# Performance work log

Measured on AMD Instinct MI355X. Metric: run time of the kernel, lower is better.

The kernel has to match this reference:

```python
import jax, jax.numpy as jnp
import numpy as np

EPS = 1e-6
ROPE_THETA = 10000.0


def setup_inputs() -> dict:
    key = jax.random.key(0)
    ks = jax.random.split(key, 6)
    B, S, D = 2, 2048, 2048
    H, KVH, HD = 16, 4, 128
    hidden_states = jax.random.normal(ks[0], (B, S, D), dtype=jnp.float32)
    # RoPE tables (HF style: freqs duplicated across the two halves)
    inv_freq = 1.0 / (ROPE_THETA ** (jnp.arange(0, HD, 2, dtype=jnp.float32) / HD))
    pos = jnp.arange(S, dtype=jnp.float32)
    freqs = pos[:, None] * inv_freq[None, :]            # [S, HD/2]
    emb = jnp.concatenate([freqs, freqs], axis=-1)       # [S, HD]
    cos, sin = jnp.cos(emb), jnp.sin(emb)
    w_scale = 0.02
    q_w = jax.random.normal(ks[1], (H * HD, D), dtype=jnp.float32) * w_scale
    k_w = jax.random.normal(ks[2], (KVH * HD, D), dtype=jnp.float32) * w_scale
    v_w = jax.random.normal(ks[3], (KVH * HD, D), dtype=jnp.float32) * w_scale
    o_w = jax.random.normal(ks[4], (D, H * HD), dtype=jnp.float32) * w_scale
    q_norm_w = jnp.ones((HD,), dtype=jnp.float32)
    k_norm_w = jnp.ones((HD,), dtype=jnp.float32)
    return {
        "hidden_states": hidden_states, "cos": cos, "sin": sin,
        "q_w": q_w, "k_w": k_w, "v_w": v_w, "o_w": o_w,
        "q_norm_w": q_norm_w, "k_norm_w": k_norm_w,
    }


def _rms_norm(x, w):
    # Qwen3RMSNorm: fp32 variance, scale, cast back
    xf = x.astype(jnp.float32)
    var = jnp.mean(xf * xf, axis=-1, keepdims=True)
    out = xf * jax.lax.rsqrt(var + EPS)
    return (out * w.astype(jnp.float32)).astype(x.dtype)


def _rotate_half(x):
    half = x.shape[-1] // 2
    return jnp.concatenate([-x[..., half:], x[..., :half]], axis=-1)


def reference(hidden_states, cos, sin, q_w, k_w, v_w, o_w, q_norm_w, k_norm_w):
    B, S, D = hidden_states.shape
    HD = q_norm_w.shape[0]
    H = q_w.shape[0] // HD
    KVH = k_w.shape[0] // HD
    groups = H // KVH
    scale = HD ** -0.5

    # QKV projections (no bias) -> [B, heads, S, HD]
    q = (hidden_states @ q_w.T).reshape(B, S, H, HD)
    k = (hidden_states @ k_w.T).reshape(B, S, KVH, HD)
    v = (hidden_states @ v_w.T).reshape(B, S, KVH, HD)
    q = _rms_norm(q, q_norm_w).transpose(0, 2, 1, 3)   # [B,H,S,HD]
    k = _rms_norm(k, k_norm_w).transpose(0, 2, 1, 3)   # [B,KVH,S,HD]
    v = v.transpose(0, 2, 1, 3)                        # [B,KVH,S,HD]

    # RoPE (broadcast over batch and heads)
    c = cos[None, None, :, :]
    s = sin[None, None, :, :]
    q = q * c + _rotate_half(q) * s
    k = k * c + _rotate_half(k) * s

    # GQA expand kv heads
    if groups > 1:
        k = jnp.repeat(k, groups, axis=1)              # [B,H,S,HD]
        v = jnp.repeat(v, groups, axis=1)

    # SDPA, non-causal, no mask, no dropout
    scores = jnp.einsum("bhqd,bhkd->bhqk", q, k) * scale
    probs = jax.nn.softmax(scores, axis=-1)
    attn = jnp.einsum("bhqk,bhkd->bhqd", probs, v)     # [B,H,S,HD]

    attn = attn.transpose(0, 2, 1, 3).reshape(B, S, H * HD)
    return attn @ o_w.T
```

## Files before the change

kernel.cpp:

```cpp
#include <hip/hip_runtime.h>
#include <hip/hip_bf16.h>
#include <math.h>

#define B_   2
#define S_   2048
#define D_   2048
#define H_   16
#define KVH_ 4
#define HD_  128
#define SCALE 0.08838834764831845f

typedef unsigned short u16;
typedef __attribute__((ext_vector_type(8))) short bf16x8;
typedef __attribute__((ext_vector_type(4))) float f32x4;

__device__ __forceinline__ u16 f2bf(float x) {
    union { float f; unsigned int u; } v; v.f = x;
    unsigned int r = v.u + 0x7fffu + ((v.u >> 16) & 1u);
    return (u16)(r >> 16);
}
__device__ __forceinline__ float bf2f(u16 b) {
    union { float f; unsigned int u; } v; v.u = ((unsigned int)b) << 16;
    return v.f;
}
__device__ __forceinline__ void gload16(const void* g, void* lds) {
    __builtin_amdgcn_global_load_lds(
        (const __attribute__((address_space(1))) unsigned int*)g,
        (__attribute__((address_space(3))) unsigned int*)lds, 16, 0, 0);
}

__global__ __launch_bounds__(256) void f2b_kernel(
    const float* __restrict__ s, u16* __restrict__ d, int n4)
{
    int i = blockIdx.x * 256 + threadIdx.x;
    if (i >= n4) return;
    float4 v = ((const float4*)s)[i];
    ushort4 o = make_ushort4(f2bf(v.x), f2bf(v.y), f2bf(v.z), f2bf(v.w));
    ((ushort4*)d)[i] = o;
}

template<int MODE>
__global__ __launch_bounds__(256) void gemm_bf16(
    const u16* __restrict__ A,
    const u16* __restrict__ Bw,
    u16* __restrict__ Qo, u16* __restrict__ Ko, u16* __restrict__ Vt,
    float* __restrict__ Co)
{
    __shared__ u16 As[128 * 64];
    __shared__ u16 Bs[128 * 64];

    const int t  = threadIdx.x;
    const int w  = t >> 6, l = t & 63;
    const int wm = w >> 1, wn = w & 1;
    const int lr = l & 15, lh = l >> 4;
    const int n0 = blockIdx.x * 128;
    const int m0 = blockIdx.y * 128;

    f32x4 acc[4][4];
    #pragma unroll
    for (int i = 0; i < 4; ++i)
        #pragma unroll
        for (int j = 0; j < 4; ++j)
            acc[i][j] = (f32x4)0.f;

    const int x  = (w * 4) * 1024 + l * 16;
    for (int k0 = 0; k0 < 2048; k0 += 64) {
        #pragma unroll
        for (int u = 0; u < 4; ++u) {
            int xb = x + u * 1024;
            int r  = xb >> 7;
            int c  = xb & 127;
            int cs = c ^ ((r & 7) << 4);
            gload16(&A[(size_t)(m0 + r) * 2048 + k0 + (cs >> 1)], &As[(w * 4 + u) * 512]);
            gload16(&Bw[(size_t)(n0 + r) * 2048 + k0 + (cs >> 1)], &Bs[(w * 4 + u) * 512]);
        }
        __syncthreads();
        #pragma unroll
        for (int kc = 0; kc < 2; ++kc) {
            bf16x8 af[4], bfr[4];
            #pragma unroll
            for (int i = 0; i < 4; ++i) {
                int row = wm * 64 + i * 16 + lr;
                int byt = row * 128 + ((kc * 64 + lh * 16) ^ ((row & 7) << 4));
                af[i] = *(const bf16x8*)&As[byt >> 1];
                int rob = wn * 64 + i * 16 + lr;
                int byb = rob * 128 + ((kc * 64 + lh * 16) ^ ((rob & 7) << 4));
                bfr[i] = *(const bf16x8*)&Bs[byb >> 1];
            }
            #pragma unroll
            for (int i = 0; i < 4; ++i)
                #pragma unroll
                for (int j = 0; j < 4; ++j)
                    acc[i][j] = __builtin_amdgcn_mfma_f32_16x16x32_bf16(
                        af[i], bfr[j], acc[i][j], 0, 0, 0);
        }
        __syncthreads();
    }

    #pragma unroll
    for (int i = 0; i < 4; ++i) {
        #pragma unroll
        for (int j = 0; j < 4; ++j) {
            int col = n0 + wn * 64 + j * 16 + lr;
            #pragma unroll
            for (int r = 0; r < 4; ++r) {
                int m = m0 + wm * 64 + i * 16 + lh * 4 + r;
                float v = acc[i][j][r];
                if (MODE == 0) {
                    int bb = m >> 11, s = m & 2047;
                    if (col < 2048) {
                        int hh = col >> 7, d = col & 127;
                        Qo[((size_t)(bb * H_ + hh) * S_ + s) * HD_ + d] = f2bf(v);
                    } else if (col < 2560) {
                        int c2 = col - 2048; int hh = c2 >> 7, d = c2 & 127;
                        Ko[((size_t)(bb * KVH_ + hh) * S_ + s) * HD_ + d] = f2bf(v);
                    } else {
                        int c2 = col - 2560; int hh = c2 >> 7, d = c2 & 127;
                        Vt[((size_t)(bb * KVH_ + hh) * HD_ + d) * S_ + s] = f2bf(v);
                    }
                } else {
                    Co[(size_t)m * 2048 + col] = v;
                }
            }
        }
    }
}

__global__ __launch_bounds__(256) void norm_rope(
    u16* __restrict__ Qb, u16* __restrict__ Kb,
    const float* __restrict__ cosb, const float* __restrict__ sinb,
    const float* __restrict__ qnw, const float* __restrict__ knw)
{
    const int rid = blockIdx.x * 4 + (threadIdx.x >> 6);
    const int l   = threadIdx.x & 63;
    u16* row; const float* wn; int s; float sc;
    if (rid < B_ * H_ * S_) {
        row = Qb + (size_t)rid * HD_; wn = qnw; s = rid & (S_ - 1); sc = SCALE;
    } else {
        int r2 = rid - B_ * H_ * S_;
        row = Kb + (size_t)r2 * HD_; wn = knw; s = r2 & (S_ - 1); sc = 1.f;
    }
    unsigned int u = *(const unsigned int*)&row[2 * l];
    float x0 = bf2f((u16)(u & 0xffff)), x1 = bf2f((u16)(u >> 16));
    float ss = x0 * x0 + x1 * x1;
    #pragma unroll
    for (int off = 1; off < 64; off <<= 1) ss += __shfl_xor(ss, off);
    float rr = rsqrtf(ss * (1.f / 128.f) + 1e-6f);
    float n0 = x0 * rr * wn[2 * l];
    float n1 = x1 * rr * wn[2 * l + 1];
    float p0 = __shfl_xor(n0, 32);
    float p1 = __shfl_xor(n1, 32);
    float sg = (l < 32) ? -1.f : 1.f;
    const float* cp = cosb + s * HD_;
    const float* sp = sinb + s * HD_;
    float o0 = (n0 * cp[2 * l]     + sg * p0 * sp[2 * l])     * sc;
    float o1 = (n1 * cp[2 * l + 1] + sg * p1 * sp[2 * l + 1]) * sc;
    unsigned int o = (unsigned int)f2bf(o0) | ((unsigned int)f2bf(o1) << 16);
    *(unsigned int*)&row[2 * l] = o;
}

__global__ __launch_bounds__(256, 2) void attn_mfma(
    const u16* __restrict__ Q,
    const u16* __restrict__ K,
    const u16* __restrict__ Vt,
    u16* __restrict__ AO)
{
    __shared__ u16 Ks[64 * 128];
    __shared__ u16 Vs[128 * 64];
    __shared__ u16 Ps[4][32 * 72];

    const int t = threadIdx.x, w = t >> 6, l = t & 63;
    const int lr = l & 15, lh = l >> 4;
    const int bh = blockIdx.y;
    const int bb = bh >> 4, h = bh & 15;
    const int kv = bb * KVH_ + (h >> 2);
    const int q0 = blockIdx.x * 128 + w * 32;

    const u16* Qp = Q + ((size_t)bh * S_ + q0) * HD_;
    const u16* Kp = K + (size_t)kv * S_ * HD_;
    const u16* Vp = Vt + (size_t)kv * HD_ * S_;

    bf16x8 aq[2][4];
    #pragma unroll
    for (int rb = 0; rb < 2; ++rb)
        #pragma unroll
        for (int dc = 0; dc < 4; ++dc)
            aq[rb][dc] = *(const bf16x8*)&Qp[(size_t)(rb * 16 + lr) * 128 + dc * 32 + lh * 8];

    f32x4 oacc[2][8];
    #pragma unroll
    for (int rb = 0; rb < 2; ++rb)
        #pragma unroll
        for (int db = 0; db < 8; ++db)
            oacc[rb][db] = (f32x4)0.f;
    float mrun[2][4], lrun[2][4];
    #pragma unroll
    for (int rb = 0; rb < 2; ++rb)
        #pragma unroll
        for (int r = 0; r < 4; ++r) { mrun[rb][r] = -1e30f; lrun[rb][r] = 0.f; }

    for (int kt = 0; kt < S_ / 64; ++kt) {
        const int k0 = kt * 64;
        #pragma unroll
        for (int u = 0; u < 4; ++u) {
            int xb = (w * 4 + u) * 1024 + l * 16;
            int rk = xb >> 8, ck = xb & 255;
            gload16(&Kp[(size_t)(k0 + rk) * 128 + ((ck ^ ((rk & 7) << 4)) >> 1)],
                    &Ks[(w * 4 + u) * 512]);
            int rv = xb >> 7, cv = xb & 127;
            gload16(&Vp[(size_t)rv * S_ + k0 + ((cv ^ ((rv & 7) << 4)) >> 1)],
                    &Vs[(w * 4 + u) * 512]);
        }
        __syncthreads();

        f32x4 sacc[2][4];
        #pragma unroll
        for (int rb = 0; rb < 2; ++rb)
            #pragma unroll
            for (int kb = 0; kb < 4; ++kb) sacc[rb][kb] = (f32x4)0.f;
        #pragma unroll
        for (int kb = 0; kb < 4; ++kb) {
            bf16x8 kf[4];
            #pragma unroll
            for (int dc = 0; dc < 4; ++dc) {
                int row = kb * 16 + lr;
                int byt = row * 256 + ((dc * 64 + lh * 16) ^ ((row & 7) << 4));
                kf[dc] = *(const bf16x8*)&Ks[byt >> 1];
            }
            #pragma unroll
            for (int rb = 0; rb < 2; ++rb)
                #pragma unroll
                for (int dc = 0; dc < 4; ++dc)
                    sacc[rb][kb] = __builtin_amdgcn_mfma_f32_16x16x32_bf16(
                        aq[rb][dc], kf[dc], sacc[rb][kb], 0, 0, 0);
        }

        #pragma unroll
        for (int rb = 0; rb < 2; ++rb) {
            #pragma unroll
            for (int r = 0; r < 4; ++r) {
                float mx = fmaxf(fmaxf(sacc[rb][0][r], sacc[rb][1][r]),
                                 fmaxf(sacc[rb][2][r], sacc[rb][3][r]));
                mx = fmaxf(mx, __shfl_xor(mx, 1));
                mx = fmaxf(mx, __shfl_xor(mx, 2));
                mx = fmaxf(mx, __shfl_xor(mx, 4));
                mx = fmaxf(mx, __shfl_xor(mx, 8));
                float mo = mrun[rb][r];
                float mn = fmaxf(mo, mx);
                float al = __expf(mo - mn);
                mrun[rb][r] = mn;
                float ps = 0.f;
                #pragma unroll
                for (int kb = 0; kb < 4; ++kb) {
                    float p = __expf(sacc[rb][kb][r] - mn);
                    sacc[rb][kb][r] = p;
                    ps += p;
                }
                ps += __shfl_xor(ps, 1);
                ps += __shfl_xor(ps, 2);
                ps += __shfl_xor(ps, 4);
                ps += __shfl_xor(ps, 8);
                lrun[rb][r] = lrun[rb][r] * al + ps;
                #pragma unroll
                for (int db = 0; db < 8; ++db)
                    oacc[rb][db][r] *= al;
                int prow = rb * 16 + lh * 4 + r;
                #pragma unroll
                for (int kb = 0; kb < 4; ++kb)
                    Ps[w][prow * 72 + kb * 16 + lr] = f2bf(sacc[rb][kb][r]);
            }
        }
        asm volatile("s_waitcnt lgkmcnt(0)" ::: "memory");

        #pragma unroll
        for (int kc = 0; kc < 2; ++kc) {
            bf16x8 pf[2];
            #pragma unroll
            for (int rb = 0; rb < 2; ++rb)
                pf[rb] = *(const bf16x8*)&Ps[w][(rb * 16 + lr) * 72 + kc * 32 + lh * 8];
            #pragma unroll
            for (int db = 0; db < 8; ++db) {
                int row = db * 16 + lr;
                int byt = row * 128 + ((kc * 64 + lh * 16) ^ ((row & 7) << 4));
                bf16x8 vf = *(const bf16x8*)&Vs[byt >> 1];
                #pragma unroll
                for (int rb = 0; rb < 2; ++rb)
                    oacc[rb][db] = __builtin_amdgcn_mfma_f32_16x16x32_bf16(
                        pf[rb], vf, oacc[rb][db], 0, 0, 0);
            }
        }
        __syncthreads();
    }

    #pragma unroll
    for (int rb = 0; rb < 2; ++rb) {
        #pragma unroll
        for (int r = 0; r < 4; ++r) {
            float inv = 1.f / lrun[rb][r];
            int s = q0 + rb * 16 + lh * 4 + r;
            size_t base = ((size_t)bb * S_ + s) * 2048 + h * 128;
            #pragma unroll
            for (int db = 0; db < 8; ++db)
                AO[base + db * 16 + lr] = f2bf(oacc[rb][db][r] * inv);
        }
    }
}

extern "C" void kernel_launch(void* const* d_in, const int* in_sizes, int n_in,
                              void* d_out, int out_size, void* d_ws, size_t ws_size,
                              hipStream_t stream) {
    (void)in_sizes; (void)n_in; (void)out_size; (void)ws_size;
    const float* hid  = (const float*)d_in[0];
    const float* cosb = (const float*)d_in[1];
    const float* sinb = (const float*)d_in[2];
    const float* qw   = (const float*)d_in[3];
    const float* kw   = (const float*)d_in[4];
    const float* vw   = (const float*)d_in[5];
    const float* ow   = (const float*)d_in[6];
    const float* qnw  = (const float*)d_in[7];
    const float* knw  = (const float*)d_in[8];

    u16* ws   = (u16*)d_ws;
    u16* hidB = ws;
    u16* Wc   = ws + 8388608;
    u16* owB  = ws + 14680064;
    u16* Qb   = ws + 18874368;
    u16* Kb   = ws + 27262976;
    u16* VtB  = ws + 29360128;
    u16* AO   = ws + 31457280;

    f2b_kernel<<<8192, 256, 0, stream>>>(hid, hidB, 2097152);
    f2b_kernel<<<4096, 256, 0, stream>>>(qw, Wc, 1048576);
    f2b_kernel<<<1024, 256, 0, stream>>>(kw, Wc + 4194304, 262144);
    f2b_kernel<<<1024, 256, 0, stream>>>(vw, Wc + 5242880, 262144);
    f2b_kernel<<<4096, 256, 0, stream>>>(ow, owB, 1048576);

    gemm_bf16<0><<<dim3(24, 32), 256, 0, stream>>>(hidB, Wc, Qb, Kb, VtB, nullptr);
    norm_rope<<<20480, 256, 0, stream>>>(Qb, Kb, cosb, sinb, qnw, knw);
    attn_mfma<<<dim3(16, 32), 256, 0, stream>>>(Qb, Kb, VtB, AO);
    gemm_bf16<1><<<dim3(16, 32), 256, 0, stream>>>(AO, owB, nullptr, nullptr, nullptr,
                                                   (float*)d_out);
}
```

Baseline: 278.0 us.

## Rewrite attention with 32x32 MFMA, register-resident P, double buffering, lazy rescale

Rebuilds the attention kernel around 32x32x16 MFMA with transposed S=K·Q^T so each lane owns one query column. P is packed to bf16 with v_cvt_pk_bf16_f32 and moved by cross-lane shuffles instead of an LDS round trip. K/V tiles are double-buffered so the next tile's loads overlap compute. Softmax works in base-2, with log2e folded into the Q scale, and skips rescaling the accumulator unless the max grows by more than 8. Block IDs are remapped to group blocks that share KV heads, at the cost of more LDS per block and higher register pressure.

```diff
diff --git a/kernel.cpp b/kernel.cpp
--- a/kernel.cpp
+++ b/kernel.cpp
@@ -9,10 +9,13 @@
 #define KVH_ 4
 #define HD_  128
 #define SCALE 0.08838834764831845f
+#define LOG2E 1.44269504088896f
 
 typedef unsigned short u16;
-typedef __attribute__((ext_vector_type(8))) short bf16x8;
-typedef __attribute__((ext_vector_type(4))) float f32x4;
+typedef unsigned int   u32;
+typedef __attribute__((ext_vector_type(8)))  short bf16x8;
+typedef __attribute__((ext_vector_type(4)))  float f32x4;
+typedef __attribute__((ext_vector_type(16))) float f32x16;
 
 __device__ __forceinline__ u16 f2bf(float x) {
     union { float f; unsigned int u; } v; v.f = x;
@@ -22,6 +25,11 @@
 __device__ __forceinline__ float bf2f(u16 b) {
     union { float f; unsigned int u; } v; v.u = ((unsigned int)b) << 16;
     return v.f;
+}
+__device__ __forceinline__ u32 cvtpk(float lo, float hi) {
+    u32 r;
+    asm("v_cvt_pk_bf16_f32 %0, %1, %2" : "=v"(r) : "v"(lo), "v"(hi));
+    return r;
 }
 __device__ __forceinline__ void gload16(const void* g, void* lds) {
     __builtin_amdgcn_global_load_lds(
@@ -135,7 +143,7 @@
     const int l   = threadIdx.x & 63;
     u16* row; const float* wn; int s; float sc;
     if (rid < B_ * H_ * S_) {
-        row = Qb + (size_t)rid * HD_; wn = qnw; s = rid & (S_ - 1); sc = SCALE;
+        row = Qb + (size_t)rid * HD_; wn = qnw; s = rid & (S_ - 1); sc = SCALE * LOG2E;
     } else {
         int r2 = rid - B_ * H_ * S_;
         row = Kb + (size_t)r2 * HD_; wn = knw; s = r2 & (S_ - 1); sc = 1.f;
@@ -165,144 +173,137 @@
     const u16* __restrict__ Vt,
     u16* __restrict__ AO)
 {
-    __shared__ u16 Ks[64 * 128];
-    __shared__ u16 Vs[128 * 64];
-    __shared__ u16 Ps[4][32 * 72];
-
-    const int t = threadIdx.x, w = t >> 6, l = t & 63;
-    const int lr = l & 15, lh = l >> 4;
-    const int bh = blockIdx.y;
+    __shared__ u16 Ks[2][64 * 128];
+    __shared__ u16 Vs[2][128 * 64];
+
+    const int t  = threadIdx.x, w = t >> 6, l = t & 63;
+    const int lq = l & 31, hi = l >> 5;
+    const int id = (blockIdx.x & 7) * 64 + (blockIdx.x >> 3);
+    const int qx = id & 15, bh = id >> 4;
     const int bb = bh >> 4, h = bh & 15;
     const int kv = bb * KVH_ + (h >> 2);
-    const int q0 = blockIdx.x * 128 + w * 32;
+    const int q0 = qx * 128 + w * 32;
 
     const u16* Qp = Q + ((size_t)bh * S_ + q0) * HD_;
     const u16* Kp = K + (size_t)kv * S_ * HD_;
     const u16* Vp = Vt + (size_t)kv * HD_ * S_;
 
-    bf16x8 aq[2][4];
-    #pragma unroll
-    for (int rb = 0; rb < 2; ++rb)
-        #pragma unroll
-        for (int dc = 0; dc < 4; ++dc)
-            aq[rb][dc] = *(const bf16x8*)&Qp[(size_t)(rb * 16 + lr) * 128 + dc * 32 + lh * 8];
-
-    f32x4 oacc[2][8];
-    #pragma unroll
-    for (int rb = 0; rb < 2; ++rb)
-        #pragma unroll
-        for (int db = 0; db < 8; ++db)
-            oacc[rb][db] = (f32x4)0.f;
-    float mrun[2][4], lrun[2][4];
-    #pragma unroll
-    for (int rb = 0; rb < 2; ++rb)
-        #pragma unroll
-        for (int r = 0; r < 4; ++r) { mrun[rb][r] = -1e30f; lrun[rb][r] = 0.f; }
-
-    for (int kt = 0; kt < S_ / 64; ++kt) {
-        const int k0 = kt * 64;
+    bf16x8 aq[8];
+    #pragma unroll
+    for (int ks = 0; ks < 8; ++ks)
+        aq[ks] = *(const bf16x8*)&Qp[(size_t)lq * 128 + ks * 16 + hi * 8];
+
+    f32x16 oacc[4];
+    #pragma unroll
+    for (int dt = 0; dt < 4; ++dt) oacc[dt] = (f32x16)0.f;
+    float mrun = -1e30f, lrun = 0.f;
+
+    auto stage = [&](int k0, int buf) {
         #pragma unroll
         for (int u = 0; u < 4; ++u) {
             int xb = (w * 4 + u) * 1024 + l * 16;
             int rk = xb >> 8, ck = xb & 255;
             gload16(&Kp[(size_t)(k0 + rk) * 128 + ((ck ^ ((rk & 7) << 4)) >> 1)],
-                    &Ks[(w * 4 + u) * 512]);
+                    &Ks[buf][(w * 4 + u) * 512]);
             int rv = xb >> 7, cv = xb & 127;
             gload16(&Vp[(size_t)rv * S_ + k0 + ((cv ^ ((rv & 7) << 4)) >> 1)],
-                    &Vs[(w * 4 + u) * 512]);
+                    &Vs[buf][(w * 4 + u) * 512]);
+        }
+    };
+
+    stage(0, 0);
+    __syncthreads();
+
+    const int NT = S_ / 64;
+    for (int kt = 0; kt < NT; ++kt) {
+        const int cur = kt & 1;
+        if (kt + 1 < NT) stage((kt + 1) * 64, cur ^ 1);
+
+        f32x16 sacc[2];
+        sacc[0] = (f32x16)0.f; sacc[1] = (f32x16)0.f;
+        #pragma unroll
+        for (int kb = 0; kb < 2; ++kb) {
+            #pragma unroll
+            for (int ks = 0; ks < 8; ++ks) {
+                int row = kb * 32 + lq;
+                int byt = row * 256 + ((ks * 32 + hi * 16) ^ ((row & 7) << 4));
+                bf16x8 kf = *(const bf16x8*)&Ks[cur][byt >> 1];
+                sacc[kb] = __builtin_amdgcn_mfma_f32_32x32x16_bf16(
+                    kf, aq[ks], sacc[kb], 0, 0, 0);
+            }
+        }
+
+        float mx = -1e30f;
+        #pragma unroll
+        for (int kb = 0; kb < 2; ++kb)
+            #pragma unroll
+            for (int r = 0; r < 16; ++r)
+                mx = fmaxf(mx, sacc[kb][r]);
+        mx = fmaxf(mx, __shfl_xor(mx, 32));
+        if (__any(mx > mrun + 8.f)) {
+            float mn = fmaxf(mrun, mx);
+            float al = __builtin_exp2f(mrun - mn);
+            mrun = mn;
+            lrun *= al;
+            #pragma unroll
+            for (int r = 0; r < 16; ++r) {
+                int src = (r & 3) + 8 * (r >> 2) + 4 * hi;
+                float alr = __shfl(al, src);
+                #pragma unroll
+                for (int dt = 0; dt < 4; ++dt) oacc[dt][r] *= alr;
+            }
+        }
+        float ps = 0.f;
+        #pragma unroll
+        for (int kb = 0; kb < 2; ++kb)
+            #pragma unroll
+            for (int r = 0; r < 16; ++r) {
+                float p = __builtin_exp2f(sacc[kb][r] - mrun);
+                sacc[kb][r] = p;
+                ps += p;
+            }
+        ps += __shfl_xor(ps, 32);
+        lrun += ps;
+
+        #pragma unroll
+        for (int kb = 0; kb < 2; ++kb) {
+            u32 wv[8], sv[8];
+            #pragma unroll
+            for (int i = 0; i < 8; ++i)
+                wv[i] = cvtpk(sacc[kb][2 * i], sacc[kb][2 * i + 1]);
+            #pragma unroll
+            for (int i = 0; i < 8; ++i)
+                sv[i] = __shfl_xor(wv[i], 32);
+            #pragma unroll
+            for (int k2 = 0; k2 < 2; ++k2) {
+                union { u32 u[4]; bf16x8 v; } pa;
+                pa.u[0] = hi ? sv[4 * k2 + 2] : wv[4 * k2 + 0];
+                pa.u[1] = hi ? sv[4 * k2 + 3] : wv[4 * k2 + 1];
+                pa.u[2] = hi ? wv[4 * k2 + 2] : sv[4 * k2 + 0];
+                pa.u[3] = hi ? wv[4 * k2 + 3] : sv[4 * k2 + 1];
+                int kloc = (kb * 2 + k2) * 16 + hi * 8;
+                #pragma unroll
+                for (int dt = 0; dt < 4; ++dt) {
+                    int rowv = dt * 32 + lq;
+                    int byv  = rowv * 128 + ((kloc * 2) ^ ((rowv & 7) << 4));
+                    bf16x8 vf = *(const bf16x8*)&Vs[cur][byv >> 1];
+                    oacc[dt] = __builtin_amdgcn_mfma_f32_32x32x16_bf16(
+                        pa.v, vf, oacc[dt], 0, 0, 0);
+                }
+            }
         }
         __syncthreads();
-
-        f32x4 sacc[2][4];
-        #pragma unroll
-        for (int rb = 0; rb < 2; ++rb)
-            #pragma unroll
-            for (int kb = 0; kb < 4; ++kb) sacc[rb][kb] = (f32x4)0.f;
-        #pragma unroll
-        for (int kb = 0; kb < 4; ++kb) {
-            bf16x8 kf[4];
-            #pragma unroll
-            for (int dc = 0; dc < 4; ++dc) {
-                int row = kb * 16 + lr;
-                int byt = row * 256 + ((dc * 64 + lh * 16) ^ ((row & 7) << 4));
-                kf[dc] = *(const bf16x8*)&Ks[byt >> 1];
-            }
-            #pragma unroll
-            for (int rb = 0; rb < 2; ++rb)
-                #pragma unroll
-                for (int dc = 0; dc < 4; ++dc)
-                    sacc[rb][kb] = __builtin_amdgcn_mfma_f32_16x16x32_bf16(
-                        aq[rb][dc], kf[dc], sacc[rb][kb], 0, 0, 0);
-        }
-
-        #pragma unroll
-        for (int rb = 0; rb < 2; ++rb) {
-            #pragma unroll
-            for (int r = 0; r < 4; ++r) {
-                float mx = fmaxf(fmaxf(sacc[rb][0][r], sacc[rb][1][r]),
-                                 fmaxf(sacc[rb][2][r], sacc[rb][3][r]));
-                mx = fmaxf(mx, __shfl_xor(mx, 1));
-                mx = fmaxf(mx, __shfl_xor(mx, 2));
-                mx = fmaxf(mx, __shfl_xor(mx, 4));
-                mx = fmaxf(mx, __shfl_xor(mx, 8));
-                float mo = mrun[rb][r];
-                float mn = fmaxf(mo, mx);
-                float al = __expf(mo - mn);
-                mrun[rb][r] = mn;
-                float ps = 0.f;
-                #pragma unroll
-                for (int kb = 0; kb < 4; ++kb) {
-                    float p = __expf(sacc[rb][kb][r] - mn);
-                    sacc[rb][kb][r] = p;
-                    ps += p;
-                }
-                ps += __shfl_xor(ps, 1);
-                ps += __shfl_xor(ps, 2);
-                ps += __shfl_xor(ps, 4);
-                ps += __shfl_xor(ps, 8);
-                lrun[rb][r] = lrun[rb][r] * al + ps;
-                #pragma unroll
-                for (int db = 0; db < 8; ++db)
-                    oacc[rb][db][r] *= al;
-                int prow = rb * 16 + lh * 4 + r;
-                #pragma unroll
-                for (int kb = 0; kb < 4; ++kb)
-                    Ps[w][prow * 72 + kb * 16 + lr] = f2bf(sacc[rb][kb][r]);
-            }
-        }
-        asm volatile("s_waitcnt lgkmcnt(0)" ::: "memory");
-
-        #pragma unroll
-        for (int kc = 0; kc < 2; ++kc) {
-            bf16x8 pf[2];
-            #pragma unroll
-            for (int rb = 0; rb < 2; ++rb)
-                pf[rb] = *(const bf16x8*)&Ps[w][(rb * 16 + lr) * 72 + kc * 32 + lh * 8];
-            #pragma unroll
-            for (int db = 0; db < 8; ++db) {
-                int row = db * 16 + lr;
-                int byt = row * 128 + ((kc * 64 + lh * 16) ^ ((row & 7) << 4));
-                bf16x8 vf = *(const bf16x8*)&Vs[byt >> 1];
-                #pragma unroll
-                for (int rb = 0; rb < 2; ++rb)
-                    oacc[rb][db] = __builtin_amdgcn_mfma_f32_16x16x32_bf16(
-                        pf[rb], vf, oacc[rb][db], 0, 0, 0);
-            }
-        }
-        __syncthreads();
-    }
-
-    #pragma unroll
-    for (int rb = 0; rb < 2; ++rb) {
-        #pragma unroll
-        for (int r = 0; r < 4; ++r) {
-            float inv = 1.f / lrun[rb][r];
-            int s = q0 + rb * 16 + lh * 4 + r;
-            size_t base = ((size_t)bb * S_ + s) * 2048 + h * 128;
-            #pragma unroll
-            for (int db = 0; db < 8; ++db)
-                AO[base + db * 16 + lr] = f2bf(oacc[rb][db][r] * inv);
-        }
+    }
+
+    #pragma unroll
+    for (int r = 0; r < 16; ++r) {
+        int src = (r & 3) + 8 * (r >> 2) + 4 * hi;
+        float linv = 1.f / __shfl(lrun, src);
+        int s = q0 + src;
+        size_t base = ((size_t)bb * S_ + s) * 2048 + h * 128 + lq;
+        #pragma unroll
+        for (int dt = 0; dt < 4; ++dt)
+            AO[base + dt * 32] = f2bf(oacc[dt][r] * linv);
     }
 }
 
@@ -337,7 +338,7 @@
 
     gemm_bf16<0><<<dim3(24, 32), 256, 0, stream>>>(hidB, Wc, Qb, Kb, VtB, nullptr);
     norm_rope<<<20480, 256, 0, stream>>>(Qb, Kb, cosb, sinb, qnw, knw);
-    attn_mfma<<<dim3(16, 32), 256, 0, stream>>>(Qb, Kb, VtB, AO);
+    attn_mfma<<<512, 256, 0, stream>>>(Qb, Kb, VtB, AO);
     gemm_bf16<1><<<dim3(16, 32), 256, 0, stream>>>(AO, owB, nullptr, nullptr, nullptr,
                                                    (float*)d_out);
 }
```

Result: faster. 242.2 us (-12.9%).
